# Optimization experiments

Measured on AMD Instinct MI355X. Metric: run time of the kernel, lower is better.

Reference implementation:

```python
import jax, jax.numpy as jnp
import numpy as np

N_NODES = 50000


def gcn_conv(x, W, src, dst, n):
    # PyG GCNConv(bias=False): h = x @ W, then symmetric-normalized
    # aggregation over A + I (self-loops added, normalize=True).
    h = x @ W  # [N, F_out]
    loop = jnp.arange(n, dtype=src.dtype)
    s = jnp.concatenate([src, loop])  # source nodes (messages come from x_j = h[s])
    d = jnp.concatenate([dst, loop])  # target nodes (aggregation index)
    ones = jnp.ones(s.shape[0], dtype=h.dtype)
    deg = jax.ops.segment_sum(ones, d, num_segments=n)  # in-degree incl. self-loop
    dinv = jnp.where(deg > 0, jax.lax.rsqrt(deg), 0.0)
    norm = dinv[s] * dinv[d]  # per-edge D^-1/2 A_hat D^-1/2 weight
    msgs = h[s] * norm[:, None]  # gather + scale
    return jax.ops.segment_sum(msgs, d, num_segments=n)  # scatter-add


def setup_inputs() -> dict:
    key = jax.random.key(0)
    k1, k2, k3, k4 = jax.random.split(key, 4)
    x = jax.random.normal(k1, (N_NODES, 256), dtype=jnp.float32)
    edge_index = jax.random.randint(k2, (2, 1600000), 0, N_NODES, dtype=jnp.int64)
    # glorot-scale weights
    W1 = jax.random.normal(k3, (256, 256), dtype=jnp.float32) * (1.0 / np.sqrt(256))
    W3 = jax.random.normal(k4, (256, 64), dtype=jnp.float32) * (1.0 / np.sqrt(256))
    return {"x": x, "edge_index": edge_index, "W1": W1, "W3": W3}


def reference(x, edge_index, W1, W3):
    n = x.shape[0]
    src, dst = edge_index[0], edge_index[1]
    h = jax.nn.relu(gcn_conv(x, W1, src, dst, n))
    h = jax.nn.relu(gcn_conv(h, W3, src, dst, n))
    return h
```

## Files before the change

kernel.cpp:

```cpp
#include <hip/hip_runtime.h>
#include <cstdint>
#include <cstddef>


#define NPART 128

__device__ __forceinline__ float bf2f(unsigned short u) {
    union { unsigned int i; float f; } c; c.i = ((unsigned int)u) << 16; return c.f;
}
__device__ __forceinline__ unsigned short f2bf(float f) {
    union { float f; unsigned int i; } c; c.f = f;
    unsigned int r = c.i + 0x7fffu + ((c.i >> 16) & 1u);
    return (unsigned short)(r >> 16);
}

__global__ __launch_bounds__(256) void wcvt_kernel(const float* __restrict__ W,
                                                   unsigned short* __restrict__ Wt,
                                                   int K, int N) {
    int idx = blockIdx.x * blockDim.x + threadIdx.x;
    if (idx < N * K) {
        int nn = idx / K, kk = idx % K;
        Wt[idx] = f2bf(W[(size_t)kk * N + nn]);
    }
}


__global__ __launch_bounds__(256) void part_hist(const int* __restrict__ dst, int E, int NB,
                                                 int* __restrict__ blockhist) {
    __shared__ int lh[1024];
    for (int t = threadIdx.x; t < NB; t += 256) lh[t] = 0;
    __syncthreads();
    const int per = (E + NPART - 1) / NPART;
    const int beg = blockIdx.x * per;
    const int end = min(E, beg + per);
    for (int i = beg + threadIdx.x; i < end; i += 256)
        atomicAdd(&lh[dst[i] >> 6], 1);
    __syncthreads();
    for (int t = threadIdx.x; t < NB; t += 256)
        blockhist[blockIdx.x * NB + t] = lh[t];
}

__global__ __launch_bounds__(1024) void part_scan(const int* __restrict__ blockhist,
                                                  int* __restrict__ bofs,
                                                  int* __restrict__ bbase, int NB) {
    __shared__ int wsum[16];
    const int t = threadIdx.x;
    const int lane = t & 63;
    int tot = 0;
    if (t < NB) {
        #pragma unroll 4
        for (int k = 0; k < NPART; ++k) tot += blockhist[k * NB + t];
    }
    int x = tot;
    #pragma unroll
    for (int off = 1; off < 64; off <<= 1) {
        int q = __shfl_up(x, off);
        if (lane >= off) x += q;
    }
    if (lane == 63) wsum[t >> 6] = x;
    __syncthreads();
    if (t < 64) {
        int y = (t < 16) ? wsum[t] : 0;
        #pragma unroll
        for (int off = 1; off < 16; off <<= 1) {
            int q = __shfl_up(y, off);
            if (lane >= off) y += q;
        }
        if (t < 16) wsum[t] = y;
    }
    __syncthreads();
    int excl = ((t >> 6) ? wsum[(t >> 6) - 1] : 0) + x - tot;
    if (t < NB) {
        bofs[t] = excl;
        if (t == NB - 1) bofs[NB] = excl + tot;
        int run = excl;
        for (int k = 0; k < NPART; ++k) {
            int c = blockhist[k * NB + t];
            bbase[k * NB + t] = run;
            run += c;
        }
    }
}

__global__ __launch_bounds__(256) void part_scatter(const int* __restrict__ src,
                                                    const int* __restrict__ dst,
                                                    const int* __restrict__ bbase,
                                                    uint2* __restrict__ pairs, int E, int NB) {
    __shared__ int lbase[1024];
    for (int t = threadIdx.x; t < NB; t += 256) lbase[t] = bbase[blockIdx.x * NB + t];
    __syncthreads();
    const int per = (E + NPART - 1) / NPART;
    const int beg = blockIdx.x * per;
    const int end = min(E, beg + per);
    for (int i = beg + threadIdx.x; i < end; i += 256) {
        int d = dst[i];
        int off = atomicAdd(&lbase[d >> 6], 1);
        pairs[off] = make_uint2((unsigned)src[i], (unsigned)d);
    }
}

__global__ __launch_bounds__(256) void bucket_build(const uint2* __restrict__ pairs,
                                                    const int* __restrict__ bofs,
                                                    int* __restrict__ rowptr,
                                                    float* __restrict__ dinv,
                                                    int* __restrict__ csr, int n) {
    const int b = blockIdx.x;
    const int node0 = b << 6;
    __shared__ int ldeg[64], lcur[64];
    if (threadIdx.x < 64) ldeg[threadIdx.x] = 0;
    __syncthreads();
    const int beg = bofs[b], end = bofs[b + 1];
    for (int i = beg + threadIdx.x; i < end; i += 256)
        atomicAdd(&ldeg[pairs[i].y & 63], 1);
    __syncthreads();
    if (threadIdx.x < 64) {
        const int lane = threadIdx.x;
        int v = ldeg[lane];
        int x = v;
        #pragma unroll
        for (int off = 1; off < 64; off <<= 1) {
            int q = __shfl_up(x, off);
            if (lane >= off) x += q;
        }
        int excl = x - v;
        int node = node0 + lane;
        if (node < n) {
            rowptr[node] = beg + excl;
            dinv[node] = rsqrtf((float)(v + 1));
        }
        lcur[lane] = beg + excl;
        if (b == (int)gridDim.x - 1 && lane == 0) rowptr[n] = end;
    }
    __syncthreads();
    for (int i = beg + threadIdx.x; i < end; i += 256) {
        uint2 p = pairs[i];
        int pos = atomicAdd(&lcur[p.y & 63], 1);
        csr[pos] = (int)p.x;
    }
}

template<int BN, int WM, int WN, bool AF32>
__global__ __launch_bounds__(256) void mfma_gemm(const void* __restrict__ Av,
                                                 const unsigned short* __restrict__ Bt,
                                                 unsigned short* __restrict__ C,
                                                 int M, int N, int K) {
    constexpr int BM = 128, BK = 64;
    constexpr int KP = 72;
    constexpr int WTM = BM / WM;
    constexpr int WTN = BN / WN;
    constexpr int MF = WTM / 16;
    constexpr int NF = WTN / 16;
    __shared__ unsigned short As[BM][KP];
    __shared__ unsigned short Bs[BN][KP];
    const int tid = threadIdx.x;
    const int wid = tid >> 6;
    const int lane = tid & 63;
    const int wr = wid / WN;
    const int wc = wid % WN;
    const int bm = blockIdx.y * BM;
    const int bn = blockIdx.x * BN;
    const int l15 = lane & 15;
    const int lg = lane >> 4;

    using bf16x8 = __attribute__((ext_vector_type(8))) short;
    using f32x4  = __attribute__((ext_vector_type(4))) float;
    f32x4 acc[MF][NF] = {};

    for (int k0 = 0; k0 < K; k0 += BK) {
        #pragma unroll
        for (int it = 0; it < (BM * BK / 8) / 256; ++it) {
            int v = tid + 256 * it;
            int row = v >> 3;
            int oct = v & 7;
            uint4 val = make_uint4(0, 0, 0, 0);
            int gr = bm + row;
            if (gr < M) {
                if (AF32) {
                    const float* A32 = (const float*)Av;
                    float4 f0 = *(const float4*)(A32 + (size_t)gr * K + k0 + oct * 8);
                    float4 f1 = *(const float4*)(A32 + (size_t)gr * K + k0 + oct * 8 + 4);
                    union { unsigned short u[8]; uint4 v4; } pk;
                    pk.u[0] = f2bf(f0.x); pk.u[1] = f2bf(f0.y);
                    pk.u[2] = f2bf(f0.z); pk.u[3] = f2bf(f0.w);
                    pk.u[4] = f2bf(f1.x); pk.u[5] = f2bf(f1.y);
                    pk.u[6] = f2bf(f1.z); pk.u[7] = f2bf(f1.w);
                    val = pk.v4;
                } else {
                    const unsigned short* Ab = (const unsigned short*)Av;
                    val = *(const uint4*)(Ab + (size_t)gr * K + k0 + oct * 8);
                }
            }
            *(uint4*)(&As[row][oct * 8]) = val;
        }
        #pragma unroll
        for (int it = 0; it < (BN * BK / 8) / 256; ++it) {
            int v = tid + 256 * it;
            int row = v >> 3;
            int oct = v & 7;
            uint4 val = *(const uint4*)(Bt + (size_t)(bn + row) * K + k0 + oct * 8);
            *(uint4*)(&Bs[row][oct * 8]) = val;
        }
        __syncthreads();
        #pragma unroll
        for (int kk = 0; kk < 2; ++kk) {
            bf16x8 af[MF], bfr[NF];
            #pragma unroll
            for (int m = 0; m < MF; ++m)
                af[m] = *(const bf16x8*)(&As[wr * WTM + m * 16 + l15][kk * 32 + lg * 8]);
            #pragma unroll
            for (int nf = 0; nf < NF; ++nf)
                bfr[nf] = *(const bf16x8*)(&Bs[wc * WTN + nf * 16 + l15][kk * 32 + lg * 8]);
            #pragma unroll
            for (int m = 0; m < MF; ++m)
                #pragma unroll
                for (int nf = 0; nf < NF; ++nf)
                    acc[m][nf] = __builtin_amdgcn_mfma_f32_16x16x32_bf16(
                        af[m], bfr[nf], acc[m][nf], 0, 0, 0);
        }
        __syncthreads();
    }
    #pragma unroll
    for (int m = 0; m < MF; ++m) {
        #pragma unroll
        for (int j = 0; j < 4; ++j) {
            int row = bm + wr * WTM + m * 16 + lg * 4 + j;
            if (row < M) {
                #pragma unroll
                for (int nf = 0; nf < NF; ++nf) {
                    int col = bn + wc * WTN + nf * 16 + l15;
                    C[(size_t)row * N + col] = f2bf(acc[m][nf][j]);
                }
            }
        }
    }
}

__global__ __launch_bounds__(256) void aggregate256_kernel(
        const unsigned short* __restrict__ h, const int* __restrict__ rowptr,
        const int* __restrict__ csr, const float* __restrict__ dinv,
        unsigned short* __restrict__ out, int n) {
    const int d = blockIdx.x;
    const int tid = threadIdx.x;
    const int wid = tid >> 6;
    const int lane = tid & 63;
    const float wd = dinv[d];
    const int beg = rowptr[d];
    const int end = rowptr[d + 1];

    float acc0 = 0.f, acc1 = 0.f, acc2 = 0.f, acc3 = 0.f;
    if (wid == 0) {
        ushort4 t = *(const ushort4*)(h + (size_t)d * 256 + lane * 4);
        float w2 = wd * wd;
        acc0 = bf2f(t.x) * w2; acc1 = bf2f(t.y) * w2;
        acc2 = bf2f(t.z) * w2; acc3 = bf2f(t.w) * w2;
    }

    __shared__ unsigned int soff[256];
    __shared__ float sw[256];
    const char* hb = (const char*)h;
    for (int k0 = beg; k0 < end; k0 += 256) {
        int cnt = min(256, end - k0);
        if (tid < cnt) {
            int s = csr[k0 + tid];
            soff[tid] = (unsigned)s * 512u;
            sw[tid] = dinv[s] * wd;
        }
        __syncthreads();
        #pragma unroll 8
        for (int e = wid; e < cnt; e += 4) {
            ushort4 t = *(const ushort4*)(hb + soff[e] + lane * 8);
            float w = sw[e];
            acc0 = fmaf(bf2f(t.x), w, acc0);
            acc1 = fmaf(bf2f(t.y), w, acc1);
            acc2 = fmaf(bf2f(t.z), w, acc2);
            acc3 = fmaf(bf2f(t.w), w, acc3);
        }
        __syncthreads();
    }

    __shared__ float part[3][256];
    if (wid > 0) {
        part[wid - 1][lane * 4 + 0] = acc0;
        part[wid - 1][lane * 4 + 1] = acc1;
        part[wid - 1][lane * 4 + 2] = acc2;
        part[wid - 1][lane * 4 + 3] = acc3;
    }
    __syncthreads();
    if (wid == 0) {
        acc0 += part[0][lane*4+0] + part[1][lane*4+0] + part[2][lane*4+0];
        acc1 += part[0][lane*4+1] + part[1][lane*4+1] + part[2][lane*4+1];
        acc2 += part[0][lane*4+2] + part[1][lane*4+2] + part[2][lane*4+2];
        acc3 += part[0][lane*4+3] + part[1][lane*4+3] + part[2][lane*4+3];
        union { unsigned short u[4]; uint2 v; } pk;
        pk.u[0] = f2bf(fmaxf(acc0, 0.f));
        pk.u[1] = f2bf(fmaxf(acc1, 0.f));
        pk.u[2] = f2bf(fmaxf(acc2, 0.f));
        pk.u[3] = f2bf(fmaxf(acc3, 0.f));
        *(uint2*)(out + (size_t)d * 256 + lane * 4) = pk.v;
    }
}

__global__ __launch_bounds__(256) void aggregate64_kernel(
        const unsigned short* __restrict__ h, const int* __restrict__ rowptr,
        const int* __restrict__ csr, const float* __restrict__ dinv,
        float* __restrict__ out, int n) {
    const int d = blockIdx.x;
    const int tid = threadIdx.x;
    const int wid = tid >> 6;
    const int lane = tid & 63;
    const float wd = dinv[d];
    const int beg = rowptr[d];
    const int end = rowptr[d + 1];

    float acc = 0.f;
    if (wid == 0) acc = bf2f(h[(size_t)d * 64 + lane]) * wd * wd;

    __shared__ unsigned int soff[256];
    __shared__ float sw[256];
    const char* hb = (const char*)h;
    for (int k0 = beg; k0 < end; k0 += 256) {
        int cnt = min(256, end - k0);
        if (tid < cnt) {
            int s = csr[k0 + tid];
            soff[tid] = (unsigned)s * 128u;
            sw[tid] = dinv[s] * wd;
        }
        __syncthreads();
        #pragma unroll 8
        for (int e = wid; e < cnt; e += 4) {
            unsigned short t = *(const unsigned short*)(hb + soff[e] + lane * 2);
            acc = fmaf(bf2f(t), sw[e], acc);
        }
        __syncthreads();
    }

    __shared__ float part[3][64];
    if (wid > 0) part[wid - 1][lane] = acc;
    __syncthreads();
    if (wid == 0) {
        acc += part[0][lane] + part[1][lane] + part[2][lane];
        out[(size_t)d * 64 + lane] = fmaxf(acc, 0.f);
    }
}


static inline size_t align256(size_t v) { return (v + 255) & ~(size_t)255; }

extern "C" void kernel_launch(void* const* d_in, const int* in_sizes, int n_in,
                              void* d_out, int out_size, void* d_ws, size_t ws_size,
                              hipStream_t stream) {
    const float* x  = (const float*)d_in[0];
    const int*   ei = (const int*)d_in[1];
    const float* W1 = (const float*)d_in[2];
    const float* W3 = (const float*)d_in[3];

    const int n = in_sizes[0] / 256;
    const int E = in_sizes[1] / 2;
    const int NB = (n + 63) >> 6;
    const int* src = ei;
    const int* dst = ei + E;

    char* w = (char*)d_ws;
    auto alloc = [&](size_t bytes) { char* p = w; w += align256(bytes); return p; };
    unsigned short* h1   = (unsigned short*)alloc((size_t)n * 256 * 2);
    unsigned short* a1   = (unsigned short*)alloc((size_t)n * 256 * 2);
    unsigned short* h2   = (unsigned short*)alloc((size_t)n * 64 * 2);
    unsigned short* W1t  = (unsigned short*)alloc(256 * 256 * 2);
    unsigned short* W3t  = (unsigned short*)alloc(64 * 256 * 2);
    float* dinv          = (float*)alloc((size_t)n * 4);
    int*   rowptr        = (int*)alloc((size_t)(n + 1) * 4);
    int*   csr           = (int*)alloc((size_t)E * 4);
    uint2* pairs         = (uint2*)alloc((size_t)E * 8);
    int*   blockhist     = (int*)alloc((size_t)NPART * NB * 4);
    int*   bbase         = (int*)alloc((size_t)NPART * NB * 4);
    int*   bofs          = (int*)alloc((size_t)(NB + 1) * 4);
    float* out           = (float*)d_out;

    wcvt_kernel<<<(256 * 256 + 255) / 256, 256, 0, stream>>>(W1, W1t, 256, 256);
    wcvt_kernel<<<(64 * 256 + 255) / 256, 256, 0, stream>>>(W3, W3t, 256, 64);

    part_hist<<<NPART, 256, 0, stream>>>(dst, E, NB, blockhist);
    part_scan<<<1, 1024, 0, stream>>>(blockhist, bofs, bbase, NB);
    part_scatter<<<NPART, 256, 0, stream>>>(src, dst, bbase, pairs, E, NB);
    bucket_build<<<NB, 256, 0, stream>>>(pairs, bofs, rowptr, dinv, csr, n);

    {
        dim3 grid(1, (n + 127) / 128);
        mfma_gemm<256, 2, 2, true><<<grid, 256, 0, stream>>>(x, W1t, h1, n, 256, 256);
        aggregate256_kernel<<<n, 256, 0, stream>>>(h1, rowptr, csr, dinv, a1, n);
    }
    {
        dim3 grid(1, (n + 127) / 128);
        mfma_gemm<64, 4, 1, false><<<grid, 256, 0, stream>>>(a1, W3t, h2, n, 64, 256);
        aggregate64_kernel<<<n, 256, 0, stream>>>(h2, rowptr, csr, dinv, out, n);
    }
}
```

Measured before the change: 313.0 us.

## Prescale GEMM rows by dinv, pack edge pairs into 32-bit words, merge weight conversions

Moves the source-side D^-1/2 scaling into the GEMM epilogue and the destination-side scaling into the aggregation epilogue. This removes the per-edge dinv gather and multiply from both aggregation kernels. Edge pairs are packed into one 32-bit word (src<<6 | dst&63), halving the intermediate buffer traffic in the CSR build; this assumes node ids fit in 26 bits. The two weight-conversion launches are merged into one kernel. Because h is scaled by dinv before rounding to bf16, rounding behaviour changes slightly.

```diff
diff --git a/kernel.cpp b/kernel.cpp
--- a/kernel.cpp
+++ b/kernel.cpp
@@ -14,13 +14,18 @@
     return (unsigned short)(r >> 16);
 }
 
-__global__ __launch_bounds__(256) void wcvt_kernel(const float* __restrict__ W,
-                                                   unsigned short* __restrict__ Wt,
-                                                   int K, int N) {
-    int idx = blockIdx.x * blockDim.x + threadIdx.x;
-    if (idx < N * K) {
-        int nn = idx / K, kk = idx % K;
-        Wt[idx] = f2bf(W[(size_t)kk * N + nn]);
+__global__ __launch_bounds__(256) void wcvt2_kernel(const float* __restrict__ W1,
+                                                    const float* __restrict__ W3,
+                                                    unsigned short* __restrict__ W1t,
+                                                    unsigned short* __restrict__ W3t) {
+    int idx = blockIdx.x * 256 + threadIdx.x;
+    if (idx < 256 * 256) {
+        int nn = idx >> 8, kk = idx & 255;
+        W1t[idx] = f2bf(W1[kk * 256 + nn]);
+    } else if (idx < 256 * 256 + 64 * 256) {
+        int j = idx - 256 * 256;
+        int nn = j >> 8, kk = j & 255;
+        W3t[j] = f2bf(W3[kk * 64 + nn]);
     }
 }
 
@@ -85,7 +90,8 @@
 __global__ __launch_bounds__(256) void part_scatter(const int* __restrict__ src,
                                                     const int* __restrict__ dst,
                                                     const int* __restrict__ bbase,
-                                                    uint2* __restrict__ pairs, int E, int NB) {
+                                                    unsigned int* __restrict__ words,
+                                                    int E, int NB) {
     __shared__ int lbase[1024];
     for (int t = threadIdx.x; t < NB; t += 256) lbase[t] = bbase[blockIdx.x * NB + t];
     __syncthreads();
@@ -95,11 +101,11 @@
     for (int i = beg + threadIdx.x; i < end; i += 256) {
         int d = dst[i];
         int off = atomicAdd(&lbase[d >> 6], 1);
-        pairs[off] = make_uint2((unsigned)src[i], (unsigned)d);
-    }
-}
-
-__global__ __launch_bounds__(256) void bucket_build(const uint2* __restrict__ pairs,
+        words[off] = ((unsigned)src[i] << 6) | (unsigned)(d & 63);
+    }
+}
+
+__global__ __launch_bounds__(256) void bucket_build(const unsigned int* __restrict__ words,
                                                     const int* __restrict__ bofs,
                                                     int* __restrict__ rowptr,
                                                     float* __restrict__ dinv,
@@ -111,7 +117,7 @@
     __syncthreads();
     const int beg = bofs[b], end = bofs[b + 1];
     for (int i = beg + threadIdx.x; i < end; i += 256)
-        atomicAdd(&ldeg[pairs[i].y & 63], 1);
+        atomicAdd(&ldeg[words[i] & 63u], 1);
     __syncthreads();
     if (threadIdx.x < 64) {
         const int lane = threadIdx.x;
@@ -133,15 +139,16 @@
     }
     __syncthreads();
     for (int i = beg + threadIdx.x; i < end; i += 256) {
-        uint2 p = pairs[i];
-        int pos = atomicAdd(&lcur[p.y & 63], 1);
-        csr[pos] = (int)p.x;
+        unsigned int w = words[i];
+        int pos = atomicAdd(&lcur[w & 63u], 1);
+        csr[pos] = (int)(w >> 6);
     }
 }
 
 template<int BN, int WM, int WN, bool AF32>
 __global__ __launch_bounds__(256) void mfma_gemm(const void* __restrict__ Av,
                                                  const unsigned short* __restrict__ Bt,
+                                                 const float* __restrict__ dinvp,
                                                  unsigned short* __restrict__ C,
                                                  int M, int N, int K) {
     constexpr int BM = 128, BK = 64;
@@ -225,10 +232,11 @@
         for (int j = 0; j < 4; ++j) {
             int row = bm + wr * WTM + m * 16 + lg * 4 + j;
             if (row < M) {
+                float s = dinvp[row];
                 #pragma unroll
                 for (int nf = 0; nf < NF; ++nf) {
                     int col = bn + wc * WTN + nf * 16 + l15;
-                    C[(size_t)row * N + col] = f2bf(acc[m][nf][j]);
+                    C[(size_t)row * N + col] = f2bf(acc[m][nf][j] * s);
                 }
             }
         }
@@ -236,44 +244,33 @@
 }
 
 __global__ __launch_bounds__(256) void aggregate256_kernel(
-        const unsigned short* __restrict__ h, const int* __restrict__ rowptr,
+        const unsigned short* __restrict__ hs, const int* __restrict__ rowptr,
         const int* __restrict__ csr, const float* __restrict__ dinv,
         unsigned short* __restrict__ out, int n) {
     const int d = blockIdx.x;
     const int tid = threadIdx.x;
     const int wid = tid >> 6;
     const int lane = tid & 63;
-    const float wd = dinv[d];
     const int beg = rowptr[d];
     const int end = rowptr[d + 1];
 
     float acc0 = 0.f, acc1 = 0.f, acc2 = 0.f, acc3 = 0.f;
     if (wid == 0) {
-        ushort4 t = *(const ushort4*)(h + (size_t)d * 256 + lane * 4);
-        float w2 = wd * wd;
-        acc0 = bf2f(t.x) * w2; acc1 = bf2f(t.y) * w2;
-        acc2 = bf2f(t.z) * w2; acc3 = bf2f(t.w) * w2;
+        ushort4 t = *(const ushort4*)(hs + (size_t)d * 256 + lane * 4);
+        acc0 = bf2f(t.x); acc1 = bf2f(t.y); acc2 = bf2f(t.z); acc3 = bf2f(t.w);
     }
 
     __shared__ unsigned int soff[256];
-    __shared__ float sw[256];
-    const char* hb = (const char*)h;
+    const char* hb = (const char*)hs;
     for (int k0 = beg; k0 < end; k0 += 256) {
         int cnt = min(256, end - k0);
-        if (tid < cnt) {
-            int s = csr[k0 + tid];
-            soff[tid] = (unsigned)s * 512u;
-            sw[tid] = dinv[s] * wd;
-        }
+        if (tid < cnt) soff[tid] = (unsigned)csr[k0 + tid] * 512u;
         __syncthreads();
         #pragma unroll 8
         for (int e = wid; e < cnt; e += 4) {
             ushort4 t = *(const ushort4*)(hb + soff[e] + lane * 8);
-            float w = sw[e];
-            acc0 = fmaf(bf2f(t.x), w, acc0);
-            acc1 = fmaf(bf2f(t.y), w, acc1);
-            acc2 = fmaf(bf2f(t.z), w, acc2);
-            acc3 = fmaf(bf2f(t.w), w, acc3);
+            acc0 += bf2f(t.x); acc1 += bf2f(t.y);
+            acc2 += bf2f(t.z); acc3 += bf2f(t.w);
         }
         __syncthreads();
     }
@@ -287,49 +284,44 @@
     }
     __syncthreads();
     if (wid == 0) {
+        const float wd = dinv[d];
         acc0 += part[0][lane*4+0] + part[1][lane*4+0] + part[2][lane*4+0];
         acc1 += part[0][lane*4+1] + part[1][lane*4+1] + part[2][lane*4+1];
         acc2 += part[0][lane*4+2] + part[1][lane*4+2] + part[2][lane*4+2];
         acc3 += part[0][lane*4+3] + part[1][lane*4+3] + part[2][lane*4+3];
         union { unsigned short u[4]; uint2 v; } pk;
-        pk.u[0] = f2bf(fmaxf(acc0, 0.f));
-        pk.u[1] = f2bf(fmaxf(acc1, 0.f));
-        pk.u[2] = f2bf(fmaxf(acc2, 0.f));
-        pk.u[3] = f2bf(fmaxf(acc3, 0.f));
+        pk.u[0] = f2bf(fmaxf(wd * acc0, 0.f));
+        pk.u[1] = f2bf(fmaxf(wd * acc1, 0.f));
+        pk.u[2] = f2bf(fmaxf(wd * acc2, 0.f));
+        pk.u[3] = f2bf(fmaxf(wd * acc3, 0.f));
         *(uint2*)(out + (size_t)d * 256 + lane * 4) = pk.v;
     }
 }
 
 __global__ __launch_bounds__(256) void aggregate64_kernel(
-        const unsigned short* __restrict__ h, const int* __restrict__ rowptr,
+        const unsigned short* __restrict__ hs, const int* __restrict__ rowptr,
         const int* __restrict__ csr, const float* __restrict__ dinv,
         float* __restrict__ out, int n) {
     const int d = blockIdx.x;
     const int tid = threadIdx.x;
     const int wid = tid >> 6;
     const int lane = tid & 63;
-    const float wd = dinv[d];
     const int beg = rowptr[d];
     const int end = rowptr[d + 1];
 
     float acc = 0.f;
-    if (wid == 0) acc = bf2f(h[(size_t)d * 64 + lane]) * wd * wd;
+    if (wid == 0) acc = bf2f(hs[(size_t)d * 64 + lane]);
 
     __shared__ unsigned int soff[256];
-    __shared__ float sw[256];
-    const char* hb = (const char*)h;
+    const char* hb = (const char*)hs;
     for (int k0 = beg; k0 < end; k0 += 256) {
         int cnt = min(256, end - k0);
-        if (tid < cnt) {
-            int s = csr[k0 + tid];
-            soff[tid] = (unsigned)s * 128u;
-            sw[tid] = dinv[s] * wd;
-        }
+        if (tid < cnt) soff[tid] = (unsigned)csr[k0 + tid] * 128u;
         __syncthreads();
         #pragma unroll 8
         for (int e = wid; e < cnt; e += 4) {
             unsigned short t = *(const unsigned short*)(hb + soff[e] + lane * 2);
-            acc = fmaf(bf2f(t), sw[e], acc);
+            acc += bf2f(t);
         }
         __syncthreads();
     }
@@ -339,7 +331,7 @@
     __syncthreads();
     if (wid == 0) {
         acc += part[0][lane] + part[1][lane] + part[2][lane];
-        out[(size_t)d * 64 + lane] = fmaxf(acc, 0.f);
+        out[(size_t)d * 64 + lane] = fmaxf(dinv[d] * acc, 0.f);
     }
 }
 
@@ -362,36 +354,35 @@
 
     char* w = (char*)d_ws;
     auto alloc = [&](size_t bytes) { char* p = w; w += align256(bytes); return p; };
-    unsigned short* h1   = (unsigned short*)alloc((size_t)n * 256 * 2);
+    unsigned short* hs1  = (unsigned short*)alloc((size_t)n * 256 * 2);
     unsigned short* a1   = (unsigned short*)alloc((size_t)n * 256 * 2);
-    unsigned short* h2   = (unsigned short*)alloc((size_t)n * 64 * 2);
+    unsigned short* hs2  = (unsigned short*)alloc((size_t)n * 64 * 2);
     unsigned short* W1t  = (unsigned short*)alloc(256 * 256 * 2);
     unsigned short* W3t  = (unsigned short*)alloc(64 * 256 * 2);
     float* dinv          = (float*)alloc((size_t)n * 4);
     int*   rowptr        = (int*)alloc((size_t)(n + 1) * 4);
     int*   csr           = (int*)alloc((size_t)E * 4);
-    uint2* pairs         = (uint2*)alloc((size_t)E * 8);
+    unsigned int* words  = (unsigned int*)alloc((size_t)E * 4);
     int*   blockhist     = (int*)alloc((size_t)NPART * NB * 4);
     int*   bbase         = (int*)alloc((size_t)NPART * NB * 4);
     int*   bofs          = (int*)alloc((size_t)(NB + 1) * 4);
     float* out           = (float*)d_out;
 
-    wcvt_kernel<<<(256 * 256 + 255) / 256, 256, 0, stream>>>(W1, W1t, 256, 256);
-    wcvt_kernel<<<(64 * 256 + 255) / 256, 256, 0, stream>>>(W3, W3t, 256, 64);
+    wcvt2_kernel<<<(256 * 256 + 64 * 256 + 255) / 256, 256, 0, stream>>>(W1, W3, W1t, W3t);
 
     part_hist<<<NPART, 256, 0, stream>>>(dst, E, NB, blockhist);
     part_scan<<<1, 1024, 0, stream>>>(blockhist, bofs, bbase, NB);
-    part_scatter<<<NPART, 256, 0, stream>>>(src, dst, bbase, pairs, E, NB);
-    bucket_build<<<NB, 256, 0, stream>>>(pairs, bofs, rowptr, dinv, csr, n);
+    part_scatter<<<NPART, 256, 0, stream>>>(src, dst, bbase, words, E, NB);
+    bucket_build<<<NB, 256, 0, stream>>>(words, bofs, rowptr, dinv, csr, n);
 
     {
         dim3 grid(1, (n + 127) / 128);
-        mfma_gemm<256, 2, 2, true><<<grid, 256, 0, stream>>>(x, W1t, h1, n, 256, 256);
-        aggregate256_kernel<<<n, 256, 0, stream>>>(h1, rowptr, csr, dinv, a1, n);
+        mfma_gemm<256, 2, 2, true><<<grid, 256, 0, stream>>>(x, W1t, dinv, hs1, n, 256, 256);
+        aggregate256_kernel<<<n, 256, 0, stream>>>(hs1, rowptr, csr, dinv, a1, n);
     }
     {
         dim3 grid(1, (n + 127) / 128);
-        mfma_gemm<64, 4, 1, false><<<grid, 256, 0, stream>>>(a1, W3t, h2, n, 64, 256);
-        aggregate64_kernel<<<n, 256, 0, stream>>>(h2, rowptr, csr, dinv, out, n);
-    }
-}
+        mfma_gemm<64, 4, 1, false><<<grid, 256, 0, stream>>>(a1, W3t, dinv, hs2, n, 64, 256);
+        aggregate64_kernel<<<n, 256, 0, stream>>>(hs2, rowptr, csr, dinv, out, n);
+    }
+}
```

Result: no change. 309.0 us, median of 2 (-1.3%).
